# Optimization experiments

Hardware: AMD Instinct MI355X
Metric: run time of the kernel (lower is better)

## Reference

```python
import jax, jax.numpy as jnp
import numpy as np

BLOCK_SIZE = 256
N_EMBD = 768
HEAD_SIZE = 768  # == n_embd so RoPE table (dim=n_embd) matches channel pairing


def _rope_tables(T, dim, theta0=10000.0):
    # compute_freq(dim=n_embd, seq_len=block_size, theta_0=10000):
    # theta_j = theta0^(-2j/dim), angle[t, j] = t * theta_j
    j = jnp.arange(dim // 2, dtype=jnp.float32)
    theta = jnp.float32(theta0) ** (-2.0 * j / jnp.float32(dim))
    ang = jnp.arange(T, dtype=jnp.float32)[:, None] * theta[None, :]  # [T, dim/2]
    return jnp.cos(ang), jnp.sin(ang)


def _apply_rope(t, cos, sin):
    # t: [B, T, D]; pair adjacent channels (2j, 2j+1) as complex, rotate.
    B, T, D = t.shape
    tr = t.reshape(B, T, D // 2, 2)
    re, im = tr[..., 0], tr[..., 1]
    out_re = re * cos[None] - im * sin[None]
    out_im = re * sin[None] + im * cos[None]
    return jnp.stack([out_re, out_im], axis=-1).reshape(B, T, D)


def setup_inputs() -> dict:
    key = jax.random.key(0)
    k1, k2, k3, k4 = jax.random.split(key, 4)
    B, T = 128, BLOCK_SIZE
    x = jax.random.normal(k1, (B, T, N_EMBD), dtype=jnp.float32)
    Wq = jax.random.normal(k2, (N_EMBD, HEAD_SIZE), dtype=jnp.float32) * 0.02
    Wk = jax.random.normal(k3, (N_EMBD, HEAD_SIZE), dtype=jnp.float32) * 0.02
    Wv = jax.random.normal(k4, (N_EMBD, HEAD_SIZE), dtype=jnp.float32) * 0.02
    return {"x": x, "Wq": Wq, "Wk": Wk, "Wv": Wv}


def reference(x, Wq, Wk, Wv):
    B, T, C = x.shape
    q = x @ Wq  # [B, T, D]
    k = x @ Wk
    v = x @ Wv
    cos, sin = _rope_tables(T, HEAD_SIZE)
    q = _apply_rope(q, cos, sin)
    k = _apply_rope(k, cos, sin)
    scale = jnp.float32(HEAD_SIZE) ** -0.5
    wei = jnp.einsum('bqd,bkd->bqk', q, k) * scale  # [B, T, T]
    causal = jnp.tril(jnp.ones((T, T), dtype=bool))
    wei = jnp.where(causal[None], wei, -jnp.inf)
    wei = jax.nn.softmax(wei, axis=-1)
    # dropout(p=0.2) is identity in eval/deterministic baseline
    out = jnp.einsum('bqk,bkd->bqd', wei, v)  # [B, T, D]
    return out
```

## Files before the change

### kernel.cpp

```cpp
#include <hip/hip_runtime.h>
#include <hip/hip_bf16.h>
#include <stdint.h>


typedef __attribute__((ext_vector_type(8))) short short8;
typedef __attribute__((ext_vector_type(4))) short short4v;
typedef __attribute__((ext_vector_type(4))) float f32x4;

__device__ __forceinline__ short f2bf(float f) {
    uint32_t u = __float_as_uint(f);
    u += 0x7fffu + ((u >> 16) & 1u);
    return (short)(u >> 16);
}

__global__ __launch_bounds__(256) void cvt_x(const float* __restrict__ x,
                                             short* __restrict__ xb) {
    long i = ((long)blockIdx.x * 256 + threadIdx.x) * 4;
    f32x4 v = *(const f32x4*)(x + i);
    short4v o;
    o.x = f2bf(v.x); o.y = f2bf(v.y); o.z = f2bf(v.z); o.w = f2bf(v.w);
    *(short4v*)(xb + i) = o;
}

__global__ __launch_bounds__(256) void cvt_wt(const float* __restrict__ W,
                                              short* __restrict__ Wt) {
    __shared__ float tile[32][33];
    int d0 = blockIdx.x * 32, c0 = blockIdx.y * 32;
    int tr = threadIdx.x >> 5, tc = threadIdx.x & 31;
    #pragma unroll
    for (int i = 0; i < 32; i += 8)
        tile[tr + i][tc] = W[(long)(c0 + tr + i) * 768 + d0 + tc];
    __syncthreads();
    #pragma unroll
    for (int i = 0; i < 32; i += 8)
        Wt[(long)(d0 + tr + i) * 768 + c0 + tc] = f2bf(tile[tc][tr + i]);
}

__global__ __launch_bounds__(256) void rope_tab(float2* __restrict__ rt) {
    int i = blockIdx.x * 256 + threadIdx.x;
    int t = i / 384, j = i - t * 384;
    const float CE = -0.034603417655f;
    float th = exp2f((float)j * CE);
    float s, c;
    sincosf((float)t * th, &s, &c);
    rt[i] = make_float2(c, s);
}

__global__ __launch_bounds__(512, 2)
void qkv256(const short* __restrict__ A, const short* __restrict__ B,
            short* __restrict__ Q, short* __restrict__ Kb,
            short* __restrict__ Vt, const float2* __restrict__ rt) {
    int p = blockIdx.x;
    int c = p & 7, j = p >> 3;
    int st = j / 9;
    int bx = j - st * 9;
    int by = c * 16 + st;
    const int m0 = by * 256, n0 = bx * 256;

    __shared__ short lA[2][256 * 64];
    __shared__ short lB[2][256 * 64];

    const int tid = threadIdx.x;
    const int w = tid >> 6, lane = tid & 63;
    const int wm = (w >> 2) * 128;
    const int wn = (w & 3) * 64;
    const int lr8 = lane >> 3;
    const int scol = (((lane & 7) - lr8) & 7) * 8;
    const int fr = lane & 15, kq = lane >> 4;

    f32x4 acc[8][4] = {};
    short8 af[4][2];
    short8 bq[4][2];

#define STAGE_HALF(lX, gX, r0g, h, t) do {                                     \
    int _buf = (t) & 1;                                                        \
    _Pragma("unroll")                                                          \
    for (int _i = 0; _i < 2; ++_i) {                                           \
        int _rl = (h) * 128 + (w * 2 + _i) * 8;                                \
        const short* _g = (gX) + (long)((r0g) + _rl + lr8) * 768               \
                               + (t) * 64 + scol;                              \
        __builtin_amdgcn_global_load_lds(                                      \
            (const __attribute__((address_space(1))) void*)_g,                 \
            (__attribute__((address_space(3))) void*)(&lX[_buf][_rl * 64]),    \
            16, 0, 0);                                                         \
    }                                                                          \
} while (0)

#define LOAD_A(mh, buf) do {                                                   \
    _Pragma("unroll")                                                          \
    for (int _t = 0; _t < 4; ++_t)                                             \
        _Pragma("unroll")                                                      \
        for (int _k = 0; _k < 2; ++_k)                                         \
            af[_t][_k] = *(const short8*)(&lA[buf][                            \
                (wm + (mh) * 64 + _t * 16 + fr) * 64 +                         \
                ((_k * 4 + kq + fr) & 7) * 8]);                                \
} while (0)

#define LOAD_B(nh, buf) do {                                                   \
    _Pragma("unroll")                                                          \
    for (int _t = 0; _t < 2; ++_t)                                             \
        _Pragma("unroll")                                                      \
        for (int _k = 0; _k < 2; ++_k)                                         \
            bq[(nh) * 2 + _t][_k] = *(const short8*)(&lB[buf][                 \
                (wn + (nh) * 32 + _t * 16 + fr) * 64 +                         \
                ((_k * 4 + kq + fr) & 7) * 8]);                                \
} while (0)

#define MMA_Q(mh, nh) do {                                                     \
    __builtin_amdgcn_s_setprio(1);                                             \
    _Pragma("unroll")                                                          \
    for (int _t = 0; _t < 4; ++_t)                                             \
        _Pragma("unroll")                                                      \
        for (int _n = 0; _n < 2; ++_n)                                         \
            _Pragma("unroll")                                                  \
            for (int _k = 0; _k < 2; ++_k)                                     \
                acc[(mh) * 4 + _t][(nh) * 2 + _n] =                            \
                    __builtin_amdgcn_mfma_f32_16x16x32_bf16(                   \
                        af[_t][_k], bq[(nh) * 2 + _n][_k],                     \
                        acc[(mh) * 4 + _t][(nh) * 2 + _n], 0, 0, 0);           \
    __builtin_amdgcn_s_setprio(0);                                             \
} while (0)

#define BAR() __builtin_amdgcn_s_barrier()
#define LGKM0() asm volatile("s_waitcnt lgkmcnt(0)" ::: "memory")
#define VMC4() asm volatile("s_waitcnt vmcnt(4)" ::: "memory")
#define VMC0() asm volatile("s_waitcnt vmcnt(0)" ::: "memory")

    STAGE_HALF(lB, B, n0, 0, 0);
    STAGE_HALF(lB, B, n0, 1, 0);
    STAGE_HALF(lA, A, m0, 0, 0);
    STAGE_HALF(lA, A, m0, 1, 0);
    STAGE_HALF(lB, B, n0, 0, 1);
    STAGE_HALF(lB, B, n0, 1, 1);
    VMC4();
    BAR();

    #pragma unroll 1
    for (int i = 0; i < 6; ++i) {
        const int t0 = 2 * i;
        const bool more = (i < 5);
        LOAD_A(0, 0); LOAD_B(0, 0);
        STAGE_HALF(lA, A, m0, 0, t0 + 1);
        BAR(); LGKM0(); MMA_Q(0, 0); BAR();
        LOAD_B(1, 0);
        STAGE_HALF(lA, A, m0, 1, t0 + 1);
        BAR(); LGKM0(); MMA_Q(0, 1); BAR();
        LOAD_A(1, 0);
        if (more) STAGE_HALF(lB, B, n0, 0, t0 + 2);
        BAR(); LGKM0(); MMA_Q(1, 1); BAR();
        if (more) STAGE_HALF(lB, B, n0, 1, t0 + 2);
        BAR(); LGKM0(); MMA_Q(1, 0);
        if (more) { VMC4(); } else { VMC0(); }
        BAR();
        LOAD_A(0, 1); LOAD_B(0, 1);
        if (more) STAGE_HALF(lA, A, m0, 0, t0 + 2);
        BAR(); LGKM0(); MMA_Q(0, 0); BAR();
        LOAD_B(1, 1);
        if (more) STAGE_HALF(lA, A, m0, 1, t0 + 2);
        BAR(); LGKM0(); MMA_Q(0, 1); BAR();
        LOAD_A(1, 1);
        if (more) STAGE_HALF(lB, B, n0, 0, t0 + 3);
        BAR(); LGKM0(); MMA_Q(1, 1); BAR();
        if (more) STAGE_HALF(lB, B, n0, 1, t0 + 3);
        BAR(); LGKM0(); MMA_Q(1, 0);
        if (more) VMC4();
        BAR();
    }

    const int type = (bx >= 6) ? 2 : (bx >= 3 ? 1 : 0);
    const int nl0 = n0 - type * 768;
    const int r0 = wm + (lane >> 4) * 4;
    const int c0 = wn + (lane & 15);
    if (type < 2) {
        short* dst = (type == 0) ? Q : Kb;
        const int par = lane & 1;
        #pragma unroll
        for (int tmi = 0; tmi < 8; ++tmi)
            #pragma unroll
            for (int tni = 0; tni < 4; ++tni) {
                int col = nl0 + c0 + tni * 16;
                const float2* rtc = rt + (col >> 1);
                #pragma unroll
                for (int r = 0; r < 4; ++r) {
                    int row = m0 + r0 + tmi * 16 + r;
                    float val = acc[tmi][tni][r];
                    float pv = __shfl_xor(val, 1);
                    float2 cs = rtc[(row & 255) * 384];
                    float re = par ? pv : val;
                    float im = par ? val : pv;
                    float o = par ? (re * cs.y + im * cs.x)
                                  : (re * cs.x - im * cs.y);
                    dst[(long)row * 768 + col] = f2bf(o);
                }
            }
    } else {
        #pragma unroll
        for (int tmi = 0; tmi < 8; ++tmi)
            #pragma unroll
            for (int tni = 0; tni < 4; ++tni) {
                int col = nl0 + c0 + tni * 16;
                #pragma unroll
                for (int r = 0; r < 4; ++r) {
                    int row = m0 + r0 + tmi * 16 + r;
                    Vt[((long)(row >> 8) * 768 + col) * 256 + (row & 255)] =
                        f2bf(acc[tmi][tni][r]);
                }
            }
    }
#undef STAGE_HALF
#undef LOAD_A
#undef LOAD_B
#undef MMA_Q
#undef BAR
#undef LGKM0
#undef VMC4
#undef VMC0
}

__global__ __launch_bounds__(256)
void attn2(const short* __restrict__ Qm, const short* __restrict__ Km,
           const short* __restrict__ Vm, float* __restrict__ out,
           float scale) {
    int p = blockIdx.x;
    int c = p & 7, j = p >> 3;
    int b = j >> 2, q0 = j & 3;
    int qh = (b & 8) ? 3 - q0 : q0;
    int bz = c * 16 + b;
    const int NC = qh + 1;
    const short* Ab = Qm + (long)bz * 196608 + (long)qh * 49152;
    const short* Bb = Km + (long)bz * 196608;
    const short* Vb = Vm + (long)bz * 196608;

    __shared__ short smem[40960];

    const int tid = threadIdx.x;
    const int w = tid >> 6, lane = tid & 63;
    const int lr8 = lane >> 3;
    const int scol = (((lane & 7) - lr8) & 7) * 8;
    const int fr = lane & 15, kq = lane >> 4;

    f32x4 acc[4][4] = {};

#define GLL(g, l) __builtin_amdgcn_global_load_lds(                            \
        (const __attribute__((address_space(1))) void*)(g),                    \
        (__attribute__((address_space(3))) void*)(l), 16, 0, 0)

#define STAGE_QK(t) do { int _b = (t) & 1;                                     \
    _Pragma("unroll")                                                          \
    for (int _i = 0; _i < 2; ++_i) { int _s = _i * 4 + w;                      \
        GLL(Ab + (long)(_s * 8 + lr8) * 768 + (t) * 64 + scol,                 \
            smem + _b * 4096 + _s * 512); }                                    \
    for (int _i = 0; _i < 2 * NC; ++_i) { int _s = _i * 4 + w;                 \
        GLL(Bb + (long)(_s * 8 + lr8) * 768 + (t) * 64 + scol,                 \
            smem + 8192 + _b * 16384 + _s * 512); } } while (0)

#define STAGE_V(dc, kc, vb) do {                                               \
    _Pragma("unroll")                                                          \
    for (int _i = 0; _i < 4; ++_i) { int _s = _i * 4 + w;                      \
        GLL(Vb + (long)((dc) * 128 + _s * 8 + lr8) * 256 + (kc) * 64 + scol,   \
            smem + 16384 + (vb) * 8192 + _s * 512); } } while (0)

    STAGE_QK(0);
    __syncthreads();
    #pragma unroll 1
    for (int t = 0; t < 12; ++t) {
        if (t < 11) STAGE_QK(t + 1);
        if (w < NC) {
            const short* la = smem + (t & 1) * 4096;
            const short* lb = smem + 8192 + (t & 1) * 16384 + w * 4096;
            #pragma unroll
            for (int cc = 0; cc < 2; ++cc) {
                const int sp = ((cc * 4 + kq + fr) & 7) * 8;
                short8 afr[4], bfr[4];
                #pragma unroll
                for (int tmi = 0; tmi < 4; ++tmi)
                    afr[tmi] = *(const short8*)(la + (tmi * 16 + fr) * 64 + sp);
                #pragma unroll
                for (int tni = 0; tni < 4; ++tni)
                    bfr[tni] = *(const short8*)(lb + (tni * 16 + fr) * 64 + sp);
                #pragma unroll
                for (int tmi = 0; tmi < 4; ++tmi)
                    #pragma unroll
                    for (int tni = 0; tni < 4; ++tni)
                        acc[tmi][tni] = __builtin_amdgcn_mfma_f32_16x16x32_bf16(
                            afr[tmi], bfr[tni], acc[tmi][tni], 0, 0, 0);
            }
        }
        __syncthreads();
    }

    STAGE_V(0, 0, 0);

    const int r0 = kq * 4;
    float* redm = (float*)(smem + 32768);
    float* reds = redm + 256;

    float M[16];
    #pragma unroll
    for (int tmi = 0; tmi < 4; ++tmi)
        #pragma unroll
        for (int r = 0; r < 4; ++r) {
            int rowL = tmi * 16 + r0 + r;
            int tloc = qh * 64 + rowL;
            float m = -1e30f;
            #pragma unroll
            for (int tni = 0; tni < 4; ++tni) {
                int col = w * 64 + fr + tni * 16;
                float v = (col <= tloc) ? acc[tmi][tni][r] * scale : -1e30f;
                acc[tmi][tni][r] = v;
                m = fmaxf(m, v);
            }
            m = fmaxf(m, __shfl_xor(m, 1));
            m = fmaxf(m, __shfl_xor(m, 2));
            m = fmaxf(m, __shfl_xor(m, 4));
            m = fmaxf(m, __shfl_xor(m, 8));
            M[tmi * 4 + r] = m;
        }
    if (fr == 0) {
        #pragma unroll
        for (int tmi = 0; tmi < 4; ++tmi)
            #pragma unroll
            for (int r = 0; r < 4; ++r)
                redm[(tmi * 16 + r0 + r) * 4 + w] = M[tmi * 4 + r];
    }
    __syncthreads();
    #pragma unroll
    for (int tmi = 0; tmi < 4; ++tmi)
        #pragma unroll
        for (int r = 0; r < 4; ++r) {
            f32x4 v = *(const f32x4*)(redm + (tmi * 16 + r0 + r) * 4);
            M[tmi * 4 + r] = fmaxf(fmaxf(v.x, v.y), fmaxf(v.z, v.w));
        }
    float Sm[16];
    #pragma unroll
    for (int tmi = 0; tmi < 4; ++tmi)
        #pragma unroll
        for (int r = 0; r < 4; ++r) {
            float mm = M[tmi * 4 + r];
            float s = 0.f;
            #pragma unroll
            for (int tni = 0; tni < 4; ++tni) {
                float e = __expf(acc[tmi][tni][r] - mm);
                acc[tmi][tni][r] = e;
                s += e;
            }
            s += __shfl_xor(s, 1);
            s += __shfl_xor(s, 2);
            s += __shfl_xor(s, 4);
            s += __shfl_xor(s, 8);
            Sm[tmi * 4 + r] = s;
        }
    if (fr == 0) {
        #pragma unroll
        for (int tmi = 0; tmi < 4; ++tmi)
            #pragma unroll
            for (int r = 0; r < 4; ++r)
                reds[(tmi * 16 + r0 + r) * 4 + w] = Sm[tmi * 4 + r];
    }
    __syncthreads();

    short* Pch = smem + w * 4096;
    #pragma unroll
    for (int tmi = 0; tmi < 4; ++tmi)
        #pragma unroll
        for (int r = 0; r < 4; ++r) {
            int rowL = tmi * 16 + r0 + r;
            f32x4 sv = *(const f32x4*)(reds + rowL * 4);
            float inv = 1.0f / (sv.x + sv.y + sv.z + sv.w);
            #pragma unroll
            for (int tni = 0; tni < 4; ++tni) {
                int l = (fr >> 3) + tni * 2;
                Pch[rowL * 64 + ((l + rowL) & 7) * 8 + (fr & 7)] =
                    f2bf(acc[tmi][tni][r] * inv);
            }
        }
    __syncthreads();

    const int wn2 = w * 32;
    const long rowB = (long)bz * 256 + (long)qh * 64;
    int vb = 0;
    #pragma unroll 1
    for (int dc = 0; dc < 6; ++dc) {
        f32x4 a2[4][2] = {};
        #pragma unroll 1
        for (int kc = 0; kc < NC; ++kc) {
            int ndc = dc, nkc = kc + 1;
            if (nkc == NC) { ndc = dc + 1; nkc = 0; }
            if (ndc < 6) STAGE_V(ndc, nkc, vb ^ 1);
            const short* pch = smem + kc * 4096;
            const short* lv = smem + 16384 + vb * 8192;
            #pragma unroll
            for (int cc = 0; cc < 2; ++cc) {
                const int sp = ((cc * 4 + kq + fr) & 7) * 8;
                short8 ap[4], bv[2];
                #pragma unroll
                for (int tmi = 0; tmi < 4; ++tmi)
                    ap[tmi] = *(const short8*)(pch + (tmi * 16 + fr) * 64 + sp);
                #pragma unroll
                for (int tn = 0; tn < 2; ++tn)
                    bv[tn] = *(const short8*)(lv + (wn2 + tn * 16 + fr) * 64 + sp);
                #pragma unroll
                for (int tmi = 0; tmi < 4; ++tmi)
                    #pragma unroll
                    for (int tn = 0; tn < 2; ++tn)
                        a2[tmi][tn] = __builtin_amdgcn_mfma_f32_16x16x32_bf16(
                            ap[tmi], bv[tn], a2[tmi][tn], 0, 0, 0);
            }
            __syncthreads();
            vb ^= 1;
        }
        #pragma unroll
        for (int tmi = 0; tmi < 4; ++tmi)
            #pragma unroll
            for (int tn = 0; tn < 2; ++tn)
                #pragma unroll
                for (int r = 0; r < 4; ++r) {
                    long row = rowB + tmi * 16 + kq * 4 + r;
                    int col = dc * 128 + wn2 + tn * 16 + fr;
                    out[row * 768 + col] = a2[tmi][tn][r];
                }
    }
#undef GLL
#undef STAGE_QK
#undef STAGE_V
}

extern "C" void kernel_launch(void* const* d_in, const int* in_sizes, int n_in,
                              void* d_out, int out_size, void* d_ws, size_t ws_size,
                              hipStream_t stream) {
    const float* x  = (const float*)d_in[0];
    const float* Wq = (const float*)d_in[1];
    const float* Wk = (const float*)d_in[2];
    const float* Wv = (const float*)d_in[3];

    char* ws = (char*)d_ws;
    short*  xb = (short*)(ws);
    short*  wt = (short*)(ws + 50331648);
    short*  qb = (short*)(ws + 53870592);
    short*  kb = (short*)(ws + 104202240);
    short*  vt = (short*)(ws + 154533888);
    float2* rt = (float2*)(ws + 255197184);

    cvt_x<<<24576, 256, 0, stream>>>(x, xb);
    dim3 gw(24, 24);
    cvt_wt<<<gw, 256, 0, stream>>>(Wq, wt);
    cvt_wt<<<gw, 256, 0, stream>>>(Wk, wt + 589824);
    cvt_wt<<<gw, 256, 0, stream>>>(Wv, wt + 1179648);
    rope_tab<<<384, 256, 0, stream>>>(rt);

    qkv256<<<1152, 512, 0, stream>>>(xb, wt, qb, kb, vt, rt);

    attn2<<<512, 256, 0, stream>>>(qb, kb, vt, (float*)d_out, 0.0360843918f);
}
```

Before: 388.3 us.

## Template attention on causal chunk count with deeper prefetch and balanced warps

The attention kernel is templated on the number of causal key chunks (NC), so the loop and accumulator bounds are compile-time. QK^T key tiles are now split evenly across all four warps instead of leaving warps idle when NC<4. Global-to-LDS staging becomes a two-deep prefetch, with explicit vmcnt waits and raw barriers replacing __syncthreads, so loads overlap MFMA work. This adds code size through four template instantiations, and the hand-counted waitcnt values are fragile and could cause races if miscounted.

```diff
diff --git a/kernel.cpp b/kernel.cpp
--- a/kernel.cpp
+++ b/kernel.cpp
@@ -217,213 +217,241 @@
 #undef VMC0
 }
 
+#define BARA() __builtin_amdgcn_s_barrier()
+#define VMW(n) asm volatile("s_waitcnt vmcnt(%0)" :: "n"(n) : "memory")
+#define LBAR() do { asm volatile("s_waitcnt lgkmcnt(0)" ::: "memory");         \
+                    __builtin_amdgcn_s_barrier(); } while (0)
+#define GLL(g, l) __builtin_amdgcn_global_load_lds(                            \
+        (const __attribute__((address_space(1))) void*)(g),                    \
+        (__attribute__((address_space(3))) void*)(l), 16, 0, 0)
+#define AQK_STAGE(t) do { int _b = (t) & 1;                                    \
+    _Pragma("unroll")                                                          \
+    for (int _i = 0; _i < 2; ++_i) { int _s = _i * 4 + w;                      \
+        GLL(Ab + (long)(_s * 8 + lr8) * 768 + (t) * 64 + scol,                 \
+            smem + _b * 4096 + _s * 512); }                                    \
+    _Pragma("unroll")                                                          \
+    for (int _i = 0; _i < 2 * NC; ++_i) { int _s = _i * 4 + w;                 \
+        GLL(Bb + (long)(_s * 8 + lr8) * 768 + (t) * 64 + scol,                 \
+            smem + 8192 + _b * 16384 + _s * 512); } } while (0)
+#define AV_STAGE(dc, kc, vb) do {                                              \
+    _Pragma("unroll")                                                          \
+    for (int _i = 0; _i < 4; ++_i) { int _s = _i * 4 + w;                      \
+        GLL(Vb + (long)((dc) * 128 + _s * 8 + lr8) * 256 + (kc) * 64 + scol,   \
+            smem + 16384 + (vb) * 8192 + _s * 512); } } while (0)
+
+template <int NC>
+__device__ __forceinline__ void attn_body(
+    int bz, int qh, const short* __restrict__ Ab, const short* __restrict__ Bb,
+    const short* __restrict__ Vb, float* __restrict__ out, float scale,
+    short* smem, int w, int lane) {
+    const int lr8 = lane >> 3;
+    const int scol = (((lane & 7) - lr8) & 7) * 8;
+    const int fr = lane & 15, kq = lane >> 4;
+    const int wNC = w * NC;
+
+    f32x4 acc[4][NC] = {};
+
+    AQK_STAGE(0);
+    AQK_STAGE(1);
+    VMW(2 + 2 * NC);
+    BARA();
+    #pragma unroll 1
+    for (int t = 0; t < 12; ++t) {
+        const short* la = smem + (t & 1) * 4096;
+        const short* lb = smem + 8192 + (t & 1) * 16384;
+        #pragma unroll
+        for (int cc = 0; cc < 2; ++cc) {
+            const int sp = ((cc * 4 + kq + fr) & 7) * 8;
+            short8 afr[4];
+            #pragma unroll
+            for (int tmi = 0; tmi < 4; ++tmi)
+                afr[tmi] = *(const short8*)(la + (tmi * 16 + fr) * 64 + sp);
+            #pragma unroll
+            for (int tni = 0; tni < NC; ++tni) {
+                short8 bfr = *(const short8*)(
+                    lb + ((wNC + tni) * 16 + fr) * 64 + sp);
+                #pragma unroll
+                for (int tmi = 0; tmi < 4; ++tmi)
+                    acc[tmi][tni] = __builtin_amdgcn_mfma_f32_16x16x32_bf16(
+                        afr[tmi], bfr, acc[tmi][tni], 0, 0, 0);
+            }
+        }
+        BARA();
+        if (t < 10) { AQK_STAGE(t + 2); VMW(2 + 2 * NC); }
+        else if (t == 10) { VMW(0); }
+        BARA();
+    }
+
+    AV_STAGE(0, 0, 0);
+    AV_STAGE(1 / NC, 1 % NC, 1);
+
+    const int r0 = kq * 4;
+    float* redm = (float*)(smem + 32768);
+    float* reds = redm + 256;
+
+    float M[16];
+    #pragma unroll
+    for (int tmi = 0; tmi < 4; ++tmi)
+        #pragma unroll
+        for (int r = 0; r < 4; ++r) {
+            int rowL = tmi * 16 + r0 + r;
+            int tloc = qh * 64 + rowL;
+            float m = -1e30f;
+            #pragma unroll
+            for (int tni = 0; tni < NC; ++tni) {
+                int col = (wNC + tni) * 16 + fr;
+                float v = (col <= tloc) ? acc[tmi][tni][r] * scale : -1e30f;
+                acc[tmi][tni][r] = v;
+                m = fmaxf(m, v);
+            }
+            m = fmaxf(m, __shfl_xor(m, 1));
+            m = fmaxf(m, __shfl_xor(m, 2));
+            m = fmaxf(m, __shfl_xor(m, 4));
+            m = fmaxf(m, __shfl_xor(m, 8));
+            M[tmi * 4 + r] = m;
+        }
+    if (fr == 0) {
+        #pragma unroll
+        for (int tmi = 0; tmi < 4; ++tmi)
+            #pragma unroll
+            for (int r = 0; r < 4; ++r)
+                redm[(tmi * 16 + r0 + r) * 4 + w] = M[tmi * 4 + r];
+    }
+    LBAR();
+    #pragma unroll
+    for (int tmi = 0; tmi < 4; ++tmi)
+        #pragma unroll
+        for (int r = 0; r < 4; ++r) {
+            f32x4 v = *(const f32x4*)(redm + (tmi * 16 + r0 + r) * 4);
+            M[tmi * 4 + r] = fmaxf(fmaxf(v.x, v.y), fmaxf(v.z, v.w));
+        }
+    float Sm[16];
+    #pragma unroll
+    for (int tmi = 0; tmi < 4; ++tmi)
+        #pragma unroll
+        for (int r = 0; r < 4; ++r) {
+            float mm = M[tmi * 4 + r];
+            float s = 0.f;
+            #pragma unroll
+            for (int tni = 0; tni < NC; ++tni) {
+                float e = __expf(acc[tmi][tni][r] - mm);
+                acc[tmi][tni][r] = e;
+                s += e;
+            }
+            s += __shfl_xor(s, 1);
+            s += __shfl_xor(s, 2);
+            s += __shfl_xor(s, 4);
+            s += __shfl_xor(s, 8);
+            Sm[tmi * 4 + r] = s;
+        }
+    if (fr == 0) {
+        #pragma unroll
+        for (int tmi = 0; tmi < 4; ++tmi)
+            #pragma unroll
+            for (int r = 0; r < 4; ++r)
+                reds[(tmi * 16 + r0 + r) * 4 + w] = Sm[tmi * 4 + r];
+    }
+    LBAR();
+
+    #pragma unroll
+    for (int tmi = 0; tmi < 4; ++tmi)
+        #pragma unroll
+        for (int r = 0; r < 4; ++r) {
+            int rowL = tmi * 16 + r0 + r;
+            f32x4 sv = *(const f32x4*)(reds + rowL * 4);
+            float inv = 1.0f / (sv.x + sv.y + sv.z + sv.w);
+            #pragma unroll
+            for (int tni = 0; tni < NC; ++tni) {
+                int ct = wNC + tni;
+                int l = (ct & 3) * 2 + (fr >> 3);
+                smem[(ct >> 2) * 4096 + rowL * 64 +
+                     ((l + rowL) & 7) * 8 + (fr & 7)] =
+                    f2bf(acc[tmi][tni][r] * inv);
+            }
+        }
+    asm volatile("s_waitcnt lgkmcnt(0)" ::: "memory");
+    VMW(4);
+    BARA();
+
+    const long rowB = (long)bz * 256 + (long)qh * 64;
+    int s = 0;
+    #pragma unroll 1
+    for (int dc = 0; dc < 6; ++dc) {
+        f32x4 a2[4][2] = {};
+        #pragma unroll 1
+        for (int kc = 0; kc < NC; ++kc, ++s) {
+            const short* pch = smem + kc * 4096;
+            const short* lv = smem + 16384 + (s & 1) * 8192;
+            #pragma unroll
+            for (int cc = 0; cc < 2; ++cc) {
+                const int sp = ((cc * 4 + kq + fr) & 7) * 8;
+                short8 ap[4], bv[2];
+                #pragma unroll
+                for (int tmi = 0; tmi < 4; ++tmi)
+                    ap[tmi] = *(const short8*)(pch + (tmi * 16 + fr) * 64 + sp);
+                #pragma unroll
+                for (int tn = 0; tn < 2; ++tn)
+                    bv[tn] = *(const short8*)(lv + (w * 32 + tn * 16 + fr) * 64 + sp);
+                #pragma unroll
+                for (int tmi = 0; tmi < 4; ++tmi)
+                    #pragma unroll
+                    for (int tn = 0; tn < 2; ++tn)
+                        a2[tmi][tn] = __builtin_amdgcn_mfma_f32_16x16x32_bf16(
+                            ap[tmi], bv[tn], a2[tmi][tn], 0, 0, 0);
+            }
+            const bool stq = (kc == NC - 1);
+            if (stq) {
+                #pragma unroll
+                for (int tmi = 0; tmi < 4; ++tmi)
+                    #pragma unroll
+                    for (int tn = 0; tn < 2; ++tn)
+                        #pragma unroll
+                        for (int r = 0; r < 4; ++r) {
+                            long row = rowB + tmi * 16 + kq * 4 + r;
+                            int col = dc * 128 + w * 32 + tn * 16 + fr;
+                            out[row * 768 + col] = a2[tmi][tn][r];
+                        }
+            }
+            BARA();
+            const int s2 = s + 2;
+            const bool pre = (s2 < 6 * NC);
+            if (pre) AV_STAGE(s2 / NC, s2 % NC, s & 1);
+            if (stq && pre)      VMW(36);
+            else if (stq)        VMW(32);
+            else if (pre)        VMW(4);
+            else                 VMW(0);
+            BARA();
+        }
+    }
+}
+
 __global__ __launch_bounds__(256)
-void attn2(const short* __restrict__ Qm, const short* __restrict__ Km,
+void attn3(const short* __restrict__ Qm, const short* __restrict__ Km,
            const short* __restrict__ Vm, float* __restrict__ out,
            float scale) {
+    __shared__ short smem[40960];
     int p = blockIdx.x;
     int c = p & 7, j = p >> 3;
     int b = j >> 2, q0 = j & 3;
     int qh = (b & 8) ? 3 - q0 : q0;
     int bz = c * 16 + b;
-    const int NC = qh + 1;
     const short* Ab = Qm + (long)bz * 196608 + (long)qh * 49152;
     const short* Bb = Km + (long)bz * 196608;
     const short* Vb = Vm + (long)bz * 196608;
-
-    __shared__ short smem[40960];
-
-    const int tid = threadIdx.x;
-    const int w = tid >> 6, lane = tid & 63;
-    const int lr8 = lane >> 3;
-    const int scol = (((lane & 7) - lr8) & 7) * 8;
-    const int fr = lane & 15, kq = lane >> 4;
-
-    f32x4 acc[4][4] = {};
-
-#define GLL(g, l) __builtin_amdgcn_global_load_lds(                            \
-        (const __attribute__((address_space(1))) void*)(g),                    \
-        (__attribute__((address_space(3))) void*)(l), 16, 0, 0)
-
-#define STAGE_QK(t) do { int _b = (t) & 1;                                     \
-    _Pragma("unroll")                                                          \
-    for (int _i = 0; _i < 2; ++_i) { int _s = _i * 4 + w;                      \
-        GLL(Ab + (long)(_s * 8 + lr8) * 768 + (t) * 64 + scol,                 \
-            smem + _b * 4096 + _s * 512); }                                    \
-    for (int _i = 0; _i < 2 * NC; ++_i) { int _s = _i * 4 + w;                 \
-        GLL(Bb + (long)(_s * 8 + lr8) * 768 + (t) * 64 + scol,                 \
-            smem + 8192 + _b * 16384 + _s * 512); } } while (0)
-
-#define STAGE_V(dc, kc, vb) do {                                               \
-    _Pragma("unroll")                                                          \
-    for (int _i = 0; _i < 4; ++_i) { int _s = _i * 4 + w;                      \
-        GLL(Vb + (long)((dc) * 128 + _s * 8 + lr8) * 256 + (kc) * 64 + scol,   \
-            smem + 16384 + (vb) * 8192 + _s * 512); } } while (0)
-
-    STAGE_QK(0);
-    __syncthreads();
-    #pragma unroll 1
-    for (int t = 0; t < 12; ++t) {
-        if (t < 11) STAGE_QK(t + 1);
-        if (w < NC) {
-            const short* la = smem + (t & 1) * 4096;
-            const short* lb = smem + 8192 + (t & 1) * 16384 + w * 4096;
-            #pragma unroll
-            for (int cc = 0; cc < 2; ++cc) {
-                const int sp = ((cc * 4 + kq + fr) & 7) * 8;
-                short8 afr[4], bfr[4];
-                #pragma unroll
-                for (int tmi = 0; tmi < 4; ++tmi)
-                    afr[tmi] = *(const short8*)(la + (tmi * 16 + fr) * 64 + sp);
-                #pragma unroll
-                for (int tni = 0; tni < 4; ++tni)
-                    bfr[tni] = *(const short8*)(lb + (tni * 16 + fr) * 64 + sp);
-                #pragma unroll
-                for (int tmi = 0; tmi < 4; ++tmi)
-                    #pragma unroll
-                    for (int tni = 0; tni < 4; ++tni)
-                        acc[tmi][tni] = __builtin_amdgcn_mfma_f32_16x16x32_bf16(
-                            afr[tmi], bfr[tni], acc[tmi][tni], 0, 0, 0);
-            }
-        }
-        __syncthreads();
-    }
-
-    STAGE_V(0, 0, 0);
-
-    const int r0 = kq * 4;
-    float* redm = (float*)(smem + 32768);
-    float* reds = redm + 256;
-
-    float M[16];
-    #pragma unroll
-    for (int tmi = 0; tmi < 4; ++tmi)
-        #pragma unroll
-        for (int r = 0; r < 4; ++r) {
-            int rowL = tmi * 16 + r0 + r;
-            int tloc = qh * 64 + rowL;
-            float m = -1e30f;
-            #pragma unroll
-            for (int tni = 0; tni < 4; ++tni) {
-                int col = w * 64 + fr + tni * 16;
-                float v = (col <= tloc) ? acc[tmi][tni][r] * scale : -1e30f;
-                acc[tmi][tni][r] = v;
-                m = fmaxf(m, v);
-            }
-            m = fmaxf(m, __shfl_xor(m, 1));
-            m = fmaxf(m, __shfl_xor(m, 2));
-            m = fmaxf(m, __shfl_xor(m, 4));
-            m = fmaxf(m, __shfl_xor(m, 8));
-            M[tmi * 4 + r] = m;
-        }
-    if (fr == 0) {
-        #pragma unroll
-        for (int tmi = 0; tmi < 4; ++tmi)
-            #pragma unroll
-            for (int r = 0; r < 4; ++r)
-                redm[(tmi * 16 + r0 + r) * 4 + w] = M[tmi * 4 + r];
-    }
-    __syncthreads();
-    #pragma unroll
-    for (int tmi = 0; tmi < 4; ++tmi)
-        #pragma unroll
-        for (int r = 0; r < 4; ++r) {
-            f32x4 v = *(const f32x4*)(redm + (tmi * 16 + r0 + r) * 4);
-            M[tmi * 4 + r] = fmaxf(fmaxf(v.x, v.y), fmaxf(v.z, v.w));
-        }
-    float Sm[16];
-    #pragma unroll
-    for (int tmi = 0; tmi < 4; ++tmi)
-        #pragma unroll
-        for (int r = 0; r < 4; ++r) {
-            float mm = M[tmi * 4 + r];
-            float s = 0.f;
-            #pragma unroll
-            for (int tni = 0; tni < 4; ++tni) {
-                float e = __expf(acc[tmi][tni][r] - mm);
-                acc[tmi][tni][r] = e;
-                s += e;
-            }
-            s += __shfl_xor(s, 1);
-            s += __shfl_xor(s, 2);
-            s += __shfl_xor(s, 4);
-            s += __shfl_xor(s, 8);
-            Sm[tmi * 4 + r] = s;
-        }
-    if (fr == 0) {
-        #pragma unroll
-        for (int tmi = 0; tmi < 4; ++tmi)
-            #pragma unroll
-            for (int r = 0; r < 4; ++r)
-                reds[(tmi * 16 + r0 + r) * 4 + w] = Sm[tmi * 4 + r];
-    }
-    __syncthreads();
-
-    short* Pch = smem + w * 4096;
-    #pragma unroll
-    for (int tmi = 0; tmi < 4; ++tmi)
-        #pragma unroll
-        for (int r = 0; r < 4; ++r) {
-            int rowL = tmi * 16 + r0 + r;
-            f32x4 sv = *(const f32x4*)(reds + rowL * 4);
-            float inv = 1.0f / (sv.x + sv.y + sv.z + sv.w);
-            #pragma unroll
-            for (int tni = 0; tni < 4; ++tni) {
-                int l = (fr >> 3) + tni * 2;
-                Pch[rowL * 64 + ((l + rowL) & 7) * 8 + (fr & 7)] =
-                    f2bf(acc[tmi][tni][r] * inv);
-            }
-        }
-    __syncthreads();
-
-    const int wn2 = w * 32;
-    const long rowB = (long)bz * 256 + (long)qh * 64;
-    int vb = 0;
-    #pragma unroll 1
-    for (int dc = 0; dc < 6; ++dc) {
-        f32x4 a2[4][2] = {};
-        #pragma unroll 1
-        for (int kc = 0; kc < NC; ++kc) {
-            int ndc = dc, nkc = kc + 1;
-            if (nkc == NC) { ndc = dc + 1; nkc = 0; }
-            if (ndc < 6) STAGE_V(ndc, nkc, vb ^ 1);
-            const short* pch = smem + kc * 4096;
-            const short* lv = smem + 16384 + vb * 8192;
-            #pragma unroll
-            for (int cc = 0; cc < 2; ++cc) {
-                const int sp = ((cc * 4 + kq + fr) & 7) * 8;
-                short8 ap[4], bv[2];
-                #pragma unroll
-                for (int tmi = 0; tmi < 4; ++tmi)
-                    ap[tmi] = *(const short8*)(pch + (tmi * 16 + fr) * 64 + sp);
-                #pragma unroll
-                for (int tn = 0; tn < 2; ++tn)
-                    bv[tn] = *(const short8*)(lv + (wn2 + tn * 16 + fr) * 64 + sp);
-                #pragma unroll
-                for (int tmi = 0; tmi < 4; ++tmi)
-                    #pragma unroll
-                    for (int tn = 0; tn < 2; ++tn)
-                        a2[tmi][tn] = __builtin_amdgcn_mfma_f32_16x16x32_bf16(
-                            ap[tmi], bv[tn], a2[tmi][tn], 0, 0, 0);
-            }
-            __syncthreads();
-            vb ^= 1;
-        }
-        #pragma unroll
-        for (int tmi = 0; tmi < 4; ++tmi)
-            #pragma unroll
-            for (int tn = 0; tn < 2; ++tn)
-                #pragma unroll
-                for (int r = 0; r < 4; ++r) {
-                    long row = rowB + tmi * 16 + kq * 4 + r;
-                    int col = dc * 128 + wn2 + tn * 16 + fr;
-                    out[row * 768 + col] = a2[tmi][tn][r];
-                }
-    }
+    int w = threadIdx.x >> 6, lane = threadIdx.x & 63;
+    switch (qh) {
+        case 0:  attn_body<1>(bz, qh, Ab, Bb, Vb, out, scale, smem, w, lane); break;
+        case 1:  attn_body<2>(bz, qh, Ab, Bb, Vb, out, scale, smem, w, lane); break;
+        case 2:  attn_body<3>(bz, qh, Ab, Bb, Vb, out, scale, smem, w, lane); break;
+        default: attn_body<4>(bz, qh, Ab, Bb, Vb, out, scale, smem, w, lane); break;
+    }
+}
+#undef BARA
+#undef VMW
+#undef LBAR
 #undef GLL
-#undef STAGE_QK
-#undef STAGE_V
-}
+#undef AQK_STAGE
+#undef AV_STAGE
 
 extern "C" void kernel_launch(void* const* d_in, const int* in_sizes, int n_in,
                               void* d_out, int out_size, void* d_ws, size_t ws_size,
@@ -450,5 +478,5 @@
 
     qkv256<<<1152, 512, 0, stream>>>(xb, wt, qb, kb, vt, rt);
 
-    attn2<<<512, 256, 0, stream>>>(qb, kb, vt, (float*)d_out, 0.0360843918f);
-}
+    attn3<<<512, 256, 0, stream>>>(qb, kb, vt, (float*)d_out, 0.0360843918f);
+}
```

Measured after the change: 412.6 us. 6.2% more time.
